# Kernel tuning notes

Hardware: AMD Instinct MI355X
Metric: run time of the kernel (lower is better)

## Reference

```python
import jax, jax.numpy as jnp
import numpy as np

EPS = 1e-6  # torch F.pairwise_distance default eps (added to diff before norm)


def setup_inputs() -> dict:
    key = jax.random.key(0)
    k1, k2 = jax.random.split(key)
    B, D, n = 4096, 1024, 64
    K = n * n
    x = jax.random.normal(k1, (B, D), dtype=jnp.float32)
    weight = jax.random.normal(k2, (D, K), dtype=jnp.float32)  # SOM codebook
    # locations = [(gx, gy) for gx in range(n) for gy in range(n)]
    gx, gy = jnp.meshgrid(jnp.arange(n), jnp.arange(n), indexing='ij')
    locations = jnp.stack([gx, gy], axis=-1).reshape(K, 2).astype(jnp.float32)
    return {"x": x, "weight": weight, "locations": locations}


def _pairwise_l2(x, weight):
    # torch: norm(x[:, :, None] - weight[None] + EPS, p=2, dim=1) -> [B, K]
    # Expanded algebraically to avoid the [B, D, K] intermediate:
    D = x.shape[1]
    x2 = jnp.sum(x * x, axis=1, keepdims=True)            # [B, 1]
    w2 = jnp.sum(weight * weight, axis=0, keepdims=True)  # [1, K]
    xw = x @ weight                                        # [B, K] GEMM
    sx = jnp.sum(x, axis=1, keepdims=True)                 # [B, 1]
    sw = jnp.sum(weight, axis=0, keepdims=True)            # [1, K]
    d2 = x2 - 2.0 * xw + w2 + 2.0 * EPS * (sx - sw) + D * EPS * EPS
    return jnp.sqrt(jnp.maximum(d2, 0.0))


def reference(x, weight, locations):
    B = x.shape[0]
    dists = _pairwise_l2(x, weight)                        # [B, K]
    losses = jnp.min(dists, axis=1, keepdims=True)         # [B, 1]
    bmu_indexes = jnp.argmin(dists, axis=1, keepdims=True)  # [B, 1] int
    bmu_locations = locations[bmu_indexes]                 # [B, 1, 2]
    loss = jnp.sum(losses) / B                             # scalar
    return bmu_locations, loss, bmu_indexes
```

## Files before the change

### kernel.cpp

```cpp
#include <hip/hip_runtime.h>

#define EPS 1e-6f

constexpr int Bn = 4096;
constexpr int Dn = 1024;
constexpr int Kn = 4096;

typedef __attribute__((ext_vector_type(8))) short short8;
typedef __attribute__((ext_vector_type(4))) float f32x4;

__device__ inline short f2bf(float f) {
    unsigned u = __float_as_uint(f);
    unsigned r = (u + 0x7FFFu + ((u >> 16) & 1u)) >> 16;
    return (short)r;
}

__device__ inline float packcand(float s, int k) {
    unsigned b = __float_as_uint(fmaxf(s, 0.5f));
    return __uint_as_float((b & 0xFFFFF000u) | (unsigned)k);
}

__global__ __launch_bounds__(256) void som_prep(
    const float* __restrict__ x, const float* __restrict__ w,
    short* __restrict__ xb, float* __restrict__ rrow,
    float* __restrict__ wtf, short* __restrict__ wt,
    float* __restrict__ cpart) {
    __shared__ float t[64][65];
    __shared__ float cp[4][64];
    __shared__ float red[8];
    const int tid = threadIdx.x;
    const int bid = blockIdx.x;
    if (bid < 2048) {
        const int lane = tid & 63, wid = tid >> 6;
        size_t i = (size_t)bid * 256 + tid;
        const float4* p = (const float4*)x;
        float4 a = p[i * 2], b = p[i * 2 + 1];
        short8 o;
        o[0] = f2bf(a.x); o[1] = f2bf(a.y); o[2] = f2bf(a.z); o[3] = f2bf(a.w);
        o[4] = f2bf(b.x); o[5] = f2bf(b.y); o[6] = f2bf(b.z); o[7] = f2bf(b.w);
        *(short8*)(xb + i * 8) = o;
        float s2 = a.x*a.x + a.y*a.y + a.z*a.z + a.w*a.w
                 + b.x*b.x + b.y*b.y + b.z*b.z + b.w*b.w;
        float s1 = a.x + a.y + a.z + a.w + b.x + b.y + b.z + b.w;
        #pragma unroll
        for (int off = 1; off < 64; off <<= 1) {
            s2 += __shfl_xor(s2, off);
            s1 += __shfl_xor(s1, off);
        }
        if (lane == 0) { red[wid] = s2; red[4 + wid] = s1; }
        __syncthreads();
        if (tid == 0)
            rrow[bid * 2] = (red[0] + red[1])
                + 2.f * EPS * (red[4] + red[5]) + (float)Dn * EPS * EPS;
        if (tid == 128)
            rrow[bid * 2 + 1] = (red[2] + red[3])
                + 2.f * EPS * (red[6] + red[7]) + (float)Dn * EPS * EPS;
    } else {
        const int tb = bid - 2048;
        const int kb = tb & 63, db = tb >> 6;
        const int k0 = kb * 64, d0 = db * 64;
        const int tx = tid & 63, ty = tid >> 6;
        #pragma unroll
        for (int i = 0; i < 16; ++i) {
            int d = i * 4 + ty;
            t[d][tx] = w[(size_t)(d0 + d) * Kn + k0 + tx];
        }
        __syncthreads();
        #pragma unroll
        for (int i = 0; i < 16; ++i) {
            int kr = i * 4 + ty;
            float v = t[tx][kr];
            wtf[(size_t)(k0 + kr) * Dn + d0 + tx] = v;
            wt [(size_t)(k0 + kr) * Dn + d0 + tx] = f2bf(v);
        }
        float cs = 0.f;
        #pragma unroll
        for (int j = 0; j < 16; ++j) {
            float v = t[ty * 16 + j][tx];
            cs = fmaf(v, v - 2.f * EPS, cs);
        }
        cp[ty][tx] = cs;
        __syncthreads();
        if (ty == 0)
            cpart[(size_t)db * Kn + k0 + tx] = cp[0][tx] + cp[1][tx] + cp[2][tx] + cp[3][tx];
    }
}

__global__ __launch_bounds__(256) void som_gemm_bf16(
    const short* __restrict__ xb, const short* __restrict__ wt,
    const float* __restrict__ cpart, float* __restrict__ pval) {
    __shared__ short As[128 * 64];
    __shared__ short Bs[128 * 64];
    const int tid = threadIdx.x;
    const int lane = tid & 63;
    const int wid = tid >> 6;
    const int wm = wid >> 1, wn = wid & 1;
    const int f = blockIdx.x;
    const int xcd = f & 7;
    const int ib = f >> 3;
    const int rb = xcd * 4 + (ib & 3);
    const int cb = ib >> 2;
    const int rowBase = rb * 128, colBase = cb * 128;

    int ldsoff[4];
    const short* gsrcA[4];
    const short* gsrcB[4];
    #pragma unroll
    for (int i = 0; i < 4; ++i) {
        int g = i * 256 + tid;
        int r = g >> 3, s = g & 7;
        ldsoff[i] = r * 64 + ((s ^ (r & 7)) << 3);
        gsrcA[i] = xb + (size_t)(rowBase + r) * Dn + s * 8;
        gsrcB[i] = wt + (size_t)(colBase + r) * Dn + s * 8;
    }

    f32x4 acc[4][4] = {};
    short8 ra[4], rbv[4];
    #pragma unroll
    for (int i = 0; i < 4; ++i) {
        ra[i]  = *(const short8*)(gsrcA[i]);
        rbv[i] = *(const short8*)(gsrcB[i]);
    }

    for (int it = 0; it < 16; ++it) {
        #pragma unroll
        for (int i = 0; i < 4; ++i) {
            *(short8*)&As[ldsoff[i]] = ra[i];
            *(short8*)&Bs[ldsoff[i]] = rbv[i];
        }
        __syncthreads();
        if (it < 15) {
            int d0 = (it + 1) * 64;
            #pragma unroll
            for (int i = 0; i < 4; ++i) {
                ra[i]  = *(const short8*)(gsrcA[i] + d0);
                rbv[i] = *(const short8*)(gsrcB[i] + d0);
            }
        }
        const int mr = wm * 64 + (lane & 15);
        const int nr = wn * 64 + (lane & 15);
        const int q = lane >> 4;
        const int lx = lane & 7;
        #pragma unroll
        for (int kk = 0; kk < 2; ++kk) {
            const int sg = (kk * 4 + q) ^ lx;
            short8 a[4], b[4];
            #pragma unroll
            for (int i = 0; i < 4; ++i) {
                a[i] = *(const short8*)&As[(mr + i * 16) * 64 + sg * 8];
                b[i] = *(const short8*)&Bs[(nr + i * 16) * 64 + sg * 8];
            }
            #pragma unroll
            for (int i = 0; i < 4; ++i)
                #pragma unroll
                for (int j = 0; j < 4; ++j)
                    acc[i][j] = __builtin_amdgcn_mfma_f32_16x16x32_bf16(
                        a[i], b[j], acc[i][j], 0, 0, 0);
        }
        __syncthreads();
    }

    const int cn = lane & 15, q = lane >> 4;
    const int nbase = colBase + wn * 64;
    float cv[4];
    #pragma unroll
    for (int j = 0; j < 4; ++j) {
        float s = 0.f;
        #pragma unroll
        for (int db = 0; db < 16; ++db)
            s += cpart[(size_t)db * Kn + nbase + j * 16 + cn];
        cv[j] = s;
    }
    #pragma unroll
    for (int i = 0; i < 4; ++i) {
        #pragma unroll
        for (int rg = 0; rg < 4; ++rg) {
            float p1 = 3.4e38f, p2 = 3.4e38f;
            #pragma unroll
            for (int j = 0; j < 4; ++j) {
                float p = packcand(fmaf(-2.f, acc[i][j][rg], cv[j]),
                                   nbase + j * 16 + cn);
                float lo = fminf(p1, p), hi = fmaxf(p1, p);
                p1 = lo; p2 = fminf(p2, hi);
            }
            #pragma unroll
            for (int off = 1; off < 16; off <<= 1) {
                float o1 = __shfl_xor(p1, off);
                float o2 = __shfl_xor(p2, off);
                float lo = fminf(p1, o1), hi = fmaxf(p1, o1);
                p1 = lo; p2 = fminf(hi, fminf(p2, o2));
            }
            if (cn == 0) {
                int mrow = rowBase + wm * 64 + i * 16 + q * 4 + rg;
                size_t e = (size_t)mrow * 128 + cb * 4 + wn * 2;
                pval[e] = p1; pval[e + 1] = p2;
            }
        }
    }
}

__global__ __launch_bounds__(256) void som_finalize(
    const float* __restrict__ x, const float* __restrict__ wtf,
    const float* __restrict__ cpart, const float* __restrict__ loc,
    const float* __restrict__ pval, const float* __restrict__ rrow,
    float* __restrict__ dist, float* __restrict__ out) {
    const int lane = threadIdx.x & 63;
    const int row = blockIdx.x * 4 + (threadIdx.x >> 6);

    const float4* xr = (const float4*)(x + (size_t)row * Dn);
    float4 xv[4];
    #pragma unroll
    for (int j = 0; j < 4; ++j) xv[j] = xr[lane * 4 + j];
    const float rrv = rrow[row];

    float v0 = pval[(size_t)row * 128 + lane];
    float v1 = pval[(size_t)row * 128 + 64 + lane];
    float g = fminf(v0, v1);
    #pragma unroll
    for (int off = 1; off < 64; off <<= 1) g = fminf(g, __shfl_xor(g, off));
    const float thr = g + 6.0f;
    unsigned long long m0 = __ballot(v0 <= thr);
    unsigned long long m1 = __ballot(v1 <= thr);

    float bestd2 = 3.4e38f; int bestk = 0x7fffffff;
    #pragma unroll
    for (int slot = 0; slot < 2; ++slot) {
        unsigned long long m = slot ? m1 : m0;
        float vs = slot ? v1 : v0;
        while (m) {
            int src = __builtin_ctzll(m); m &= m - 1;
            int k = ((int)__float_as_uint(__shfl(vs, src))) & 0xFFF;
            const float4* wr = (const float4*)(wtf + (size_t)k * Dn);
            float dt = 0.f;
            #pragma unroll
            for (int j = 0; j < 4; ++j) {
                float4 wv = wr[lane * 4 + j];
                dt += xv[j].x * wv.x + xv[j].y * wv.y + xv[j].z * wv.z + xv[j].w * wv.w;
            }
            #pragma unroll
            for (int off = 1; off < 64; off <<= 1) dt += __shfl_xor(dt, off);
            float ck = 0.f;
            #pragma unroll
            for (int db = 0; db < 16; ++db) ck += cpart[(size_t)db * Kn + k];
            float d2 = rrv + ck - 2.f * dt;
            if (d2 < bestd2 || (d2 == bestd2 && k < bestk)) { bestd2 = d2; bestk = k; }
        }
    }
    if (lane == 0) {
        out[2 * row]     = loc[2 * bestk];
        out[2 * row + 1] = loc[2 * bestk + 1];
        out[8193 + row]  = (float)bestk;
        dist[row]        = sqrtf(fmaxf(bestd2, 0.f));
    }
}

__global__ __launch_bounds__(256) void som_loss(const float* __restrict__ dist,
                                                float* __restrict__ out) {
    __shared__ float red[4];
    const int tid = threadIdx.x;
    const int lane = tid & 63, wid = tid >> 6;
    const float4* p = (const float4*)dist;
    float s = 0.f;
    #pragma unroll
    for (int j = 0; j < 4; ++j) {
        float4 v = p[tid + j * 256];
        s += v.x + v.y + v.z + v.w;
    }
    #pragma unroll
    for (int off = 1; off < 64; off <<= 1) s += __shfl_xor(s, off);
    if (lane == 0) red[wid] = s;
    __syncthreads();
    if (tid == 0)
        out[8192] = (red[0] + red[1] + red[2] + red[3]) * (1.0f / (float)Bn);
}

extern "C" void kernel_launch(void* const* d_in, const int* in_sizes, int n_in,
                              void* d_out, int out_size, void* d_ws, size_t ws_size,
                              hipStream_t stream) {
    const float* x   = (const float*)d_in[0];
    const float* w   = (const float*)d_in[1];
    const float* loc = (const float*)d_in[2];
    float* out = (float*)d_out;

    float* rrow = (float*)d_ws;
    float* wtf  = rrow + Bn;
    short* wt   = (short*)(wtf + (size_t)Kn * Dn);
    short* xb   = wt + (size_t)Kn * Dn;
    float* pval = (float*)(xb + (size_t)Bn * Dn);
    float* cpart = pval + (size_t)Bn * 128;
    float* dist  = cpart + 16 * Kn;

    som_prep<<<3072, 256, 0, stream>>>(x, w, xb, rrow, wtf, wt, cpart);
    som_gemm_bf16<<<1024, 256, 0, stream>>>(xb, wt, cpart, pval);
    som_finalize<<<Bn / 4, 256, 0, stream>>>(x, wtf, cpart, loc, pval, rrow, dist, out);
    som_loss<<<1, 256, 0, stream>>>(dist, out);
}
```

Measured before the change: 144.1 us.

## Switch candidate-screening GEMM from bf16 to fp8 MFMA with wider refine threshold

Quantizes x and the transposed codebook to fp8 instead of bf16, and runs the screening GEMM with fp8 16x16x32 MFMAs over 128-wide K tiles in a padded LDS layout. This halves operand bytes and the number of K iterations. Because fp8 scores are noisier, the finalize kernel's candidate threshold is widened from +6 to +30, so more candidates get the exact fp32 recheck. The layout uses row padding instead of an XOR swizzle, and the added launch-bounds occupancy hint may affect register allocation.

```diff
diff --git a/kernel.cpp b/kernel.cpp
--- a/kernel.cpp
+++ b/kernel.cpp
@@ -6,13 +6,14 @@
 constexpr int Dn = 1024;
 constexpr int Kn = 4096;
 
-typedef __attribute__((ext_vector_type(8))) short short8;
 typedef __attribute__((ext_vector_type(4))) float f32x4;
-
-__device__ inline short f2bf(float f) {
-    unsigned u = __float_as_uint(f);
-    unsigned r = (u + 0x7FFFu + ((u >> 16) & 1u)) >> 16;
-    return (short)r;
+typedef __attribute__((ext_vector_type(2))) long long ll2;
+
+__device__ inline int pk_fp8_lo(float a, float b, int old) {
+    return __builtin_amdgcn_cvt_pk_fp8_f32(a, b, old, false);
+}
+__device__ inline int pk_fp8_hi(float a, float b, int old) {
+    return __builtin_amdgcn_cvt_pk_fp8_f32(a, b, old, true);
 }
 
 __device__ inline float packcand(float s, int k) {
@@ -22,8 +23,8 @@
 
 __global__ __launch_bounds__(256) void som_prep(
     const float* __restrict__ x, const float* __restrict__ w,
-    short* __restrict__ xb, float* __restrict__ rrow,
-    float* __restrict__ wtf, short* __restrict__ wt,
+    unsigned char* __restrict__ xf8, float* __restrict__ rrow,
+    float* __restrict__ wtf, unsigned char* __restrict__ wf8,
     float* __restrict__ cpart) {
     __shared__ float t[64][65];
     __shared__ float cp[4][64];
@@ -35,10 +36,9 @@
         size_t i = (size_t)bid * 256 + tid;
         const float4* p = (const float4*)x;
         float4 a = p[i * 2], b = p[i * 2 + 1];
-        short8 o;
-        o[0] = f2bf(a.x); o[1] = f2bf(a.y); o[2] = f2bf(a.z); o[3] = f2bf(a.w);
-        o[4] = f2bf(b.x); o[5] = f2bf(b.y); o[6] = f2bf(b.z); o[7] = f2bf(b.w);
-        *(short8*)(xb + i * 8) = o;
+        int lo = pk_fp8_lo(a.x, a.y, 0); lo = pk_fp8_hi(a.z, a.w, lo);
+        int hi = pk_fp8_lo(b.x, b.y, 0); hi = pk_fp8_hi(b.z, b.w, hi);
+        ((int2*)xf8)[i] = make_int2(lo, hi);
         float s2 = a.x*a.x + a.y*a.y + a.z*a.z + a.w*a.w
                  + b.x*b.x + b.y*b.y + b.z*b.z + b.w*b.w;
         float s1 = a.x + a.y + a.z + a.w + b.x + b.y + b.z + b.w;
@@ -71,7 +71,8 @@
             int kr = i * 4 + ty;
             float v = t[tx][kr];
             wtf[(size_t)(k0 + kr) * Dn + d0 + tx] = v;
-            wt [(size_t)(k0 + kr) * Dn + d0 + tx] = f2bf(v);
+            wf8[(size_t)(k0 + kr) * Dn + d0 + tx] =
+                (unsigned char)(pk_fp8_lo(v, v, 0) & 0xFF);
         }
         float cs = 0.f;
         #pragma unroll
@@ -86,11 +87,11 @@
     }
 }
 
-__global__ __launch_bounds__(256) void som_gemm_bf16(
-    const short* __restrict__ xb, const short* __restrict__ wt,
+__global__ __launch_bounds__(256, 3) void som_gemm_fp8(
+    const unsigned char* __restrict__ xf8, const unsigned char* __restrict__ wf8,
     const float* __restrict__ cpart, float* __restrict__ pval) {
-    __shared__ short As[128 * 64];
-    __shared__ short Bs[128 * 64];
+    __shared__ __align__(16) unsigned char As[128 * 144];
+    __shared__ __align__(16) unsigned char Bs[128 * 144];
     const int tid = threadIdx.x;
     const int lane = tid & 63;
     const int wid = tid >> 6;
@@ -102,60 +103,64 @@
     const int cb = ib >> 2;
     const int rowBase = rb * 128, colBase = cb * 128;
 
-    int ldsoff[4];
-    const short* gsrcA[4];
-    const short* gsrcB[4];
+    int offA[4];
+    const unsigned char* gsrcA[4];
+    const unsigned char* gsrcB[4];
     #pragma unroll
     for (int i = 0; i < 4; ++i) {
         int g = i * 256 + tid;
         int r = g >> 3, s = g & 7;
-        ldsoff[i] = r * 64 + ((s ^ (r & 7)) << 3);
-        gsrcA[i] = xb + (size_t)(rowBase + r) * Dn + s * 8;
-        gsrcB[i] = wt + (size_t)(colBase + r) * Dn + s * 8;
+        offA[i] = r * 144 + (2 * (s & 1)) * 32 + (s >> 1) * 8;
+        gsrcA[i] = xf8 + (size_t)(rowBase + r) * Dn + s * 16;
+        gsrcB[i] = wf8 + (size_t)(colBase + r) * Dn + s * 16;
     }
 
     f32x4 acc[4][4] = {};
-    short8 ra[4], rbv[4];
+    ll2 ra[4], rbv[4];
     #pragma unroll
     for (int i = 0; i < 4; ++i) {
-        ra[i]  = *(const short8*)(gsrcA[i]);
-        rbv[i] = *(const short8*)(gsrcB[i]);
-    }
-
-    for (int it = 0; it < 16; ++it) {
+        ra[i]  = *(const ll2*)(gsrcA[i]);
+        rbv[i] = *(const ll2*)(gsrcB[i]);
+    }
+
+    const int mrA = (wm * 64 + (lane & 15)) * 144;
+    const int nrB = (wn * 64 + (lane & 15)) * 144;
+    const int qoff = (lane >> 4) * 32;
+
+    for (int it = 0; it < 8; ++it) {
         #pragma unroll
         for (int i = 0; i < 4; ++i) {
-            *(short8*)&As[ldsoff[i]] = ra[i];
-            *(short8*)&Bs[ldsoff[i]] = rbv[i];
-        }
-        __syncthreads();
-        if (it < 15) {
-            int d0 = (it + 1) * 64;
+            *(long long*)&As[offA[i]]      = ra[i][0];
+            *(long long*)&As[offA[i] + 32] = ra[i][1];
+            *(long long*)&Bs[offA[i]]      = rbv[i][0];
+            *(long long*)&Bs[offA[i] + 32] = rbv[i][1];
+        }
+        __syncthreads();
+        if (it < 7) {
+            int d0 = (it + 1) * 128;
             #pragma unroll
             for (int i = 0; i < 4; ++i) {
-                ra[i]  = *(const short8*)(gsrcA[i] + d0);
-                rbv[i] = *(const short8*)(gsrcB[i] + d0);
-            }
-        }
-        const int mr = wm * 64 + (lane & 15);
-        const int nr = wn * 64 + (lane & 15);
-        const int q = lane >> 4;
-        const int lx = lane & 7;
-        #pragma unroll
-        for (int kk = 0; kk < 2; ++kk) {
-            const int sg = (kk * 4 + q) ^ lx;
-            short8 a[4], b[4];
+                ra[i]  = *(const ll2*)(gsrcA[i] + d0);
+                rbv[i] = *(const ll2*)(gsrcB[i] + d0);
+            }
+        }
+        #pragma unroll
+        for (int kk2 = 0; kk2 < 2; ++kk2) {
+            ll2 a2[4], b2[4];
             #pragma unroll
             for (int i = 0; i < 4; ++i) {
-                a[i] = *(const short8*)&As[(mr + i * 16) * 64 + sg * 8];
-                b[i] = *(const short8*)&Bs[(nr + i * 16) * 64 + sg * 8];
+                a2[i] = *(const ll2*)&As[mrA + i * 16 * 144 + qoff + kk2 * 16];
+                b2[i] = *(const ll2*)&Bs[nrB + i * 16 * 144 + qoff + kk2 * 16];
             }
             #pragma unroll
             for (int i = 0; i < 4; ++i)
                 #pragma unroll
-                for (int j = 0; j < 4; ++j)
-                    acc[i][j] = __builtin_amdgcn_mfma_f32_16x16x32_bf16(
-                        a[i], b[j], acc[i][j], 0, 0, 0);
+                for (int j = 0; j < 4; ++j) {
+                    acc[i][j] = __builtin_amdgcn_mfma_f32_16x16x32_fp8_fp8(
+                        a2[i][0], b2[j][0], acc[i][j], 0, 0, 0);
+                    acc[i][j] = __builtin_amdgcn_mfma_f32_16x16x32_fp8_fp8(
+                        a2[i][1], b2[j][1], acc[i][j], 0, 0, 0);
+                }
         }
         __syncthreads();
     }
@@ -218,7 +223,7 @@
     float g = fminf(v0, v1);
     #pragma unroll
     for (int off = 1; off < 64; off <<= 1) g = fminf(g, __shfl_xor(g, off));
-    const float thr = g + 6.0f;
+    const float thr = g + 30.0f;
     unsigned long long m0 = __ballot(v0 <= thr);
     unsigned long long m1 = __ballot(v1 <= thr);
 
@@ -284,14 +289,14 @@
 
     float* rrow = (float*)d_ws;
     float* wtf  = rrow + Bn;
-    short* wt   = (short*)(wtf + (size_t)Kn * Dn);
-    short* xb   = wt + (size_t)Kn * Dn;
-    float* pval = (float*)(xb + (size_t)Bn * Dn);
+    unsigned char* wf8 = (unsigned char*)(wtf + (size_t)Kn * Dn);
+    unsigned char* xf8 = wf8 + (size_t)Kn * Dn;
+    float* pval = (float*)(xf8 + (size_t)Bn * Dn);
     float* cpart = pval + (size_t)Bn * 128;
     float* dist  = cpart + 16 * Kn;
 
-    som_prep<<<3072, 256, 0, stream>>>(x, w, xb, rrow, wtf, wt, cpart);
-    som_gemm_bf16<<<1024, 256, 0, stream>>>(xb, wt, cpart, pval);
+    som_prep<<<3072, 256, 0, stream>>>(x, w, xf8, rrow, wtf, wf8, cpart);
+    som_gemm_fp8<<<1024, 256, 0, stream>>>(xf8, wf8, cpart, pval);
     som_finalize<<<Bn / 4, 256, 0, stream>>>(x, wtf, cpart, loc, pval, rrow, dist, out);
     som_loss<<<1, 256, 0, stream>>>(dist, out);
 }
```

New measurement: 142.0 us (median of 2 runs). Within noise of the previous version (-1.4%).
